# Kernel optimization log

Hardware: AMD Instinct MI355X
Metric: run time of the kernel (lower is better)

## Reference

```python
import jax, jax.numpy as jnp
import numpy as np

D_MODEL = 1024
NUM_HEADS = 16
D_K = D_MODEL // NUM_HEADS


def setup_inputs() -> dict:
    key = jax.random.key(0)
    ks = jax.random.split(key, 11)
    B, T = 4, 2048
    s = 1.0 / np.sqrt(D_MODEL)
    return {
        'query': jax.random.normal(ks[0], (B, T, D_MODEL), jnp.float32),
        'key': jax.random.normal(ks[1], (B, T, D_MODEL), jnp.float32),
        'value': jax.random.normal(ks[2], (B, T, D_MODEL), jnp.float32),
        'Wq': jax.random.normal(ks[3], (D_MODEL, D_MODEL), jnp.float32) * s,
        'bq': jnp.zeros((D_MODEL,), jnp.float32),
        'Wk': jax.random.normal(ks[4], (D_MODEL, D_MODEL), jnp.float32) * s,
        'bk': jnp.zeros((D_MODEL,), jnp.float32),
        'Wv': jax.random.normal(ks[5], (D_MODEL, D_MODEL), jnp.float32) * s,
        'bv': jnp.zeros((D_MODEL,), jnp.float32),
        'Wo': jax.random.normal(ks[6], (D_MODEL, D_MODEL), jnp.float32) * s,
        'bo': jnp.zeros((D_MODEL,), jnp.float32),
    }


def reference(query, key, value, Wq, bq, Wk, bk, Wv, bv, Wo, bo):
    B, Tq, _ = query.shape
    Tk = key.shape[1]
    # projections (torch Linear: x @ W.T + b)
    q = (query @ Wq.T + bq).reshape(B, Tq, NUM_HEADS, D_K).transpose(0, 2, 1, 3)
    k = (key @ Wk.T + bk).reshape(B, Tk, NUM_HEADS, D_K).transpose(0, 2, 1, 3)
    v = (value @ Wv.T + bv).reshape(B, Tk, NUM_HEADS, D_K).transpose(0, 2, 1, 3)
    scale = 1.0 / jnp.sqrt(jnp.asarray(D_K, q.dtype))
    scores = jnp.einsum('bhqd,bhkd->bhqk', q, k) * scale  # [B,H,Tq,Tk]
    attn = jax.nn.softmax(scores, axis=-1)
    out = jnp.einsum('bhqk,bhkd->bhqd', attn, v)
    out = out.transpose(0, 2, 1, 3).reshape(B, Tq, D_MODEL)
    return out @ Wo.T + bo
```

## Files before the change

### kernel.cpp

```cpp
#include <hip/hip_runtime.h>

typedef unsigned short u16;
typedef unsigned int u32;
typedef __attribute__((ext_vector_type(8))) short bf16x8;
typedef __attribute__((ext_vector_type(4))) float f32x4;

__device__ inline u16 f2bf(float x) {
  union { float f; unsigned u; } v; v.f = x;
  unsigned r = v.u + 0x7fffu + ((v.u >> 16) & 1u);
  return (u16)(r >> 16);
}

__device__ inline u32 packbf2(float p0, float p1) {
  return __builtin_amdgcn_perm(__float_as_uint(p1), __float_as_uint(p0), 0x07060302u);
}

__device__ inline void gload16(const void* g, void* l) {
  __builtin_amdgcn_global_load_lds(
      (const __attribute__((address_space(1))) unsigned int*)g,
      (__attribute__((address_space(3))) unsigned int*)l,
      16, 0, 0);
}

__global__ void cvt_all(const float* __restrict__ q, const float* __restrict__ k,
                        const float* __restrict__ v,
                        const float* __restrict__ wq, const float* __restrict__ wk,
                        const float* __restrict__ wv, const float* __restrict__ wo,
                        u16* __restrict__ ws) {
  const size_t MT4 = (size_t)2 * 1024 * 1024;
  const int i = blockIdx.x * blockDim.x + threadIdx.x;
  const int t = blockIdx.y;
  float4 vv;
  ushort4 o;
  if (t < 3) {
    const float* src = (t == 0) ? q : (t == 1) ? k : v;
    vv = ((const float4*)src)[i];
    o.x = f2bf(vv.x); o.y = f2bf(vv.y); o.z = f2bf(vv.z); o.w = f2bf(vv.w);
    ((ushort4*)ws)[(size_t)t * MT4 + i] = o;
  } else {
    if (i >= (1 << 20)) return;
    const int w = i >> 18, j = i & 0x3FFFF;
    const float* src = (w == 0) ? wq : (w == 1) ? wk : (w == 2) ? wv : wo;
    vv = ((const float4*)src)[j];
    o.x = f2bf(vv.x); o.y = f2bf(vv.y); o.z = f2bf(vv.z); o.w = f2bf(vv.w);
    ((ushort4*)(ws + 3 * MT4 * 4))[i] = o;
  }
}

__global__ __launch_bounds__(256, 3) void gemm_qkv(
    const u16* __restrict__ Xq, const u16* __restrict__ Wqb,
    const float* __restrict__ bq_, const float* __restrict__ bk_,
    const float* __restrict__ bv_, u16* __restrict__ Qp)
{
  constexpr int N = 1024, K = 1024, BK = 32, NT = K / BK;
  constexpr size_t MT = (size_t)8192 * 1024, WT = (size_t)1024 * 1024;
  __shared__ __align__(16) u16 As[2][128 * BK];
  __shared__ __align__(16) u16 Bs[2][128 * BK];
  const int z = blockIdx.z;
  const u16* A = Xq + (size_t)z * MT;
  const u16* W = Wqb + (size_t)z * WT;
  const float* bias = (z == 0) ? bq_ : (z == 1) ? bk_ : bv_;
  u16* Cout = Qp + (size_t)z * MT;
  const bool vm = (z == 2);

  const int tid = threadIdx.x;
  const int wave = tid >> 6, lane = tid & 63;
  const int quad = lane >> 4, l16 = lane & 15;
  const int m0 = blockIdx.x * 128, n0 = blockIdx.y * 128;

  const int sA = wave * 2;
  const int srow = lane >> 2;
  const int skcol = ((lane & 3) ^ (srow & 3)) * 8;
  const int mloc = sA * 16 + srow;
  const int arow = vm ? ((mloc & 64) + (mloc & 3) * 16 + ((mloc & 63) >> 2)) : mloc;
  const int astep = vm ? 4 : 16;
  const u16* ag = A + (size_t)(m0 + arow) * K + skcol;
  const u16* bg = W + (size_t)(n0 + mloc) * K + skcol;

  const int wm = (wave >> 1) * 64, wn = (wave & 1) * 64;
  f32x4 acc[4][4] = {};

  gload16(ag, As[0] + sA * 512);
  gload16(ag + (size_t)astep * K, As[0] + sA * 512 + 512);
  gload16(bg, Bs[0] + sA * 512);
  gload16(bg + 16 * K, Bs[0] + sA * 512 + 512);
  ag += BK; bg += BK;
  __syncthreads();

  int cur = 0;
  for (int kt = 0; kt < NT; ++kt) {
    if (kt + 1 < NT) {
      const int nb = cur ^ 1;
      gload16(ag, As[nb] + sA * 512);
      gload16(ag + (size_t)astep * K, As[nb] + sA * 512 + 512);
      gload16(bg, Bs[nb] + sA * 512);
      gload16(bg + 16 * K, Bs[nb] + sA * 512 + 512);
      ag += BK; bg += BK;
    }
    const u16* Ac = As[cur];
    const u16* Bc = Bs[cur];
    bf16x8 af[4], bf[4];
#pragma unroll
    for (int mi = 0; mi < 4; ++mi)
      af[mi] = *(const bf16x8*)(Ac + (wm + mi * 16 + l16) * BK + ((quad ^ (l16 & 3)) * 8));
#pragma unroll
    for (int ni = 0; ni < 4; ++ni)
      bf[ni] = *(const bf16x8*)(Bc + (wn + ni * 16 + l16) * BK + ((quad ^ (l16 & 3)) * 8));
#pragma unroll
    for (int mi = 0; mi < 4; ++mi)
#pragma unroll
      for (int ni = 0; ni < 4; ++ni)
        acc[mi][ni] = __builtin_amdgcn_mfma_f32_16x16x32_bf16(af[mi], bf[ni], acc[mi][ni], 0, 0, 0);
    __syncthreads();
    cur ^= 1;
  }

#pragma unroll
  for (int ni = 0; ni < 4; ++ni) {
    const int col = n0 + wn + ni * 16 + l16;
    const float bv = bias[col];
#pragma unroll
    for (int mi = 0; mi < 4; ++mi) {
      const int mrow = m0 + wm + mi * 16 + quad * 4;
      f32x4 a = acc[mi][ni];
      if (!vm) {
#pragma unroll
        for (int r = 0; r < 4; ++r)
          Cout[(size_t)(mrow + r) * N + col] = f2bf(a[r] + bv);
      } else {
        const int bq = mrow >> 11, t = mrow & 2047;
        const int h = col >> 6, d = col & 63;
        ushort4 pk;
        pk.x = f2bf(a[0] + bv); pk.y = f2bf(a[1] + bv);
        pk.z = f2bf(a[2] + bv); pk.w = f2bf(a[3] + bv);
        *(ushort4*)(Cout + ((size_t)((bq * 16 + h) * 64 + d)) * 2048 + t) = pk;
      }
    }
  }
}

template<int MODE>
__global__ __launch_bounds__(256, 2) void gemm_bt(
    const u16* __restrict__ A, const u16* __restrict__ W,
    const float* __restrict__ bias, void* __restrict__ Cout)
{
  constexpr int N = 1024, K = 1024, BK = 32, NT = K / BK;
  __shared__ __align__(16) u16 As[2][128 * BK];
  __shared__ __align__(16) u16 Bs[2][128 * BK];
  const int tid = threadIdx.x;
  const int wave = tid >> 6, lane = tid & 63;
  const int quad = lane >> 4, l16 = lane & 15;
  const int m0 = blockIdx.x * 128, n0 = blockIdx.y * 128;

  const int sA = wave * 2;
  const int srow = lane >> 2;
  const int skcol = ((lane & 3) ^ (srow & 3)) * 8;
  const int mloc = sA * 16 + srow;
  const u16* ag = A + (size_t)(m0 + mloc) * K + skcol;
  const u16* bg = W + (size_t)(n0 + mloc) * K + skcol;

  const int wm = (wave >> 1) * 64, wn = (wave & 1) * 64;
  f32x4 acc[4][4] = {};

  gload16(ag, As[0] + sA * 512);
  gload16(ag + 16 * K, As[0] + sA * 512 + 512);
  gload16(bg, Bs[0] + sA * 512);
  gload16(bg + 16 * K, Bs[0] + sA * 512 + 512);
  ag += BK; bg += BK;
  __syncthreads();

  int cur = 0;
  for (int kt = 0; kt < NT; ++kt) {
    if (kt + 1 < NT) {
      const int nb = cur ^ 1;
      gload16(ag, As[nb] + sA * 512);
      gload16(ag + 16 * K, As[nb] + sA * 512 + 512);
      gload16(bg, Bs[nb] + sA * 512);
      gload16(bg + 16 * K, Bs[nb] + sA * 512 + 512);
      ag += BK; bg += BK;
    }
    const u16* Ac = As[cur];
    const u16* Bc = Bs[cur];
    bf16x8 af[4], bf[4];
#pragma unroll
    for (int mi = 0; mi < 4; ++mi)
      af[mi] = *(const bf16x8*)(Ac + (wm + mi * 16 + l16) * BK + ((quad ^ (l16 & 3)) * 8));
#pragma unroll
    for (int ni = 0; ni < 4; ++ni)
      bf[ni] = *(const bf16x8*)(Bc + (wn + ni * 16 + l16) * BK + ((quad ^ (l16 & 3)) * 8));
#pragma unroll
    for (int mi = 0; mi < 4; ++mi)
#pragma unroll
      for (int ni = 0; ni < 4; ++ni)
        acc[mi][ni] = __builtin_amdgcn_mfma_f32_16x16x32_bf16(af[mi], bf[ni], acc[mi][ni], 0, 0, 0);
    __syncthreads();
    cur ^= 1;
  }

#pragma unroll
  for (int ni = 0; ni < 4; ++ni) {
    const int col = n0 + wn + ni * 16 + l16;
    const float bv = bias[col];
#pragma unroll
    for (int mi = 0; mi < 4; ++mi) {
      const int mrow = m0 + wm + mi * 16 + quad * 4;
      f32x4 a = acc[mi][ni];
      float* C = (float*)Cout;
#pragma unroll
      for (int r = 0; r < 4; ++r)
        C[(size_t)(mrow + r) * N + col] = a[r] + bv;
    }
  }
}

__global__ __launch_bounds__(512, 4) void flash_attn(
    const u16* __restrict__ Qp, const u16* __restrict__ Kp,
    const u16* __restrict__ Vt, u16* __restrict__ Ctx)
{
  constexpr int TQ = 2048, DM = 1024, DK = 64;
  __shared__ __align__(16) u16 Ks[2][128 * 64];
  __shared__ __align__(16) u16 Vts[2][64 * 128];
  __shared__ __align__(16) u16 Ps[8][16 * 64];

  const int bh = blockIdx.x, b = bh >> 4, h = bh & 15;
  const int qt = blockIdx.y;
  const int tid = threadIdx.x, wave = tid >> 6, lane = tid & 63;
  const int quad = lane >> 4, l16 = lane & 15;
  const int q0 = qt * 256 + wave * 32;

  const int C0 = tid, C1 = 512 + tid;
  const int kr0 = C0 >> 3, kr1 = C1 >> 3;
  const u16* kp0 = Kp + (size_t)(b * TQ + kr0) * DM + h * DK + (((C0 & 7) ^ (kr0 & 7)) * 8);
  const u16* kp1 = Kp + (size_t)(b * TQ + kr1) * DM + h * DK + (((C1 & 7) ^ (kr1 & 7)) * 8);
  const int vd0 = C0 >> 4, vd1 = C1 >> 4;
  const u16* vp0 = Vt + (size_t)(bh * DK + vd0) * TQ + (((C0 & 15) ^ (vd0 & 15)) * 8);
  const u16* vp1 = Vt + (size_t)(bh * DK + vd1) * TQ + (((C1 & 15) ^ (vd1 & 15)) * 8);

  bf16x8 qf[2][2];
#pragma unroll
  for (int mi = 0; mi < 2; ++mi)
#pragma unroll
    for (int ks = 0; ks < 2; ++ks)
      qf[mi][ks] = *(const bf16x8*)(Qp + (size_t)(b * TQ + q0 + mi * 16 + l16) * DM
                                       + h * DK + ks * 32 + quad * 8);

  f32x4 O[2][4] = {};
  f32x4 lsum[2] = {};
  const float CS = 0.18033688011112042f;
  const float CB = 0.0028153f;

  bf16x8 onesv;
#pragma unroll
  for (int j = 0; j < 8; ++j) onesv[j] = (short)0x3F80;

  gload16(kp0, &Ks[0][C0 * 8]);
  gload16(kp1, &Ks[0][C1 * 8]);
  gload16(vp0, &Vts[0][C0 * 8]);
  gload16(vp1, &Vts[0][C1 * 8]);
  kp0 += 128 * DM; kp1 += 128 * DM; vp0 += 128; vp1 += 128;
  __syncthreads();

  const int kg = quad ^ (l16 & 7);
  int cur = 0;
  for (int kt = 0; kt < TQ / 128; ++kt) {
    if (kt + 1 < TQ / 128) {
      const int nb = cur ^ 1;
      gload16(kp0, &Ks[nb][C0 * 8]);
      gload16(kp1, &Ks[nb][C1 * 8]);
      gload16(vp0, &Vts[nb][C0 * 8]);
      gload16(vp1, &Vts[nb][C1 * 8]);
      kp0 += 128 * DM; kp1 += 128 * DM; vp0 += 128; vp1 += 128;
    }
    const u16* Kc = Ks[cur];
    const u16* Vc = Vts[cur];
    u16* Psw = Ps[wave];

#pragma unroll
    for (int g = 0; g < 2; ++g) {
      f32x4 Sg[2][4];
      __builtin_amdgcn_s_setprio(1);
#pragma unroll
      for (int cc = 0; cc < 4; ++cc) {
        const int row = (g * 4 + cc) * 16 + l16;
        bf16x8 kf0 = *(const bf16x8*)(Kc + row * 64 + kg * 8);
        bf16x8 kf1 = *(const bf16x8*)(Kc + row * 64 + (kg ^ 4) * 8);
#pragma unroll
        for (int mi = 0; mi < 2; ++mi) {
          f32x4 zz = {};
          zz = __builtin_amdgcn_mfma_f32_16x16x32_bf16(qf[mi][0], kf0, zz, 0, 0, 0);
          Sg[mi][cc] = __builtin_amdgcn_mfma_f32_16x16x32_bf16(qf[mi][1], kf1, zz, 0, 0, 0);
        }
      }
      __builtin_amdgcn_s_setprio(0);
      bf16x8 pf[2][2];
#pragma unroll
      for (int mi = 0; mi < 2; ++mi) {
#pragma unroll
        for (int r = 0; r < 4; ++r) {
          float e0 = __builtin_amdgcn_exp2f(fmaf(Sg[mi][0][r], CS, CB));
          float e1 = __builtin_amdgcn_exp2f(fmaf(Sg[mi][1][r], CS, CB));
          float e2 = __builtin_amdgcn_exp2f(fmaf(Sg[mi][2][r], CS, CB));
          float e3 = __builtin_amdgcn_exp2f(fmaf(Sg[mi][3][r], CS, CB));
          uint2 pk;
          pk.x = packbf2(e0, e1);
          pk.y = packbf2(e2, e3);
          const int pw = quad * 4 + r;
          *(uint2*)(&Psw[pw * 64 + ((l16 * 4) ^ ((pw & 7) << 3))]) = pk;
        }
#pragma unroll
        for (int ksl = 0; ksl < 2; ++ksl)
          pf[mi][ksl] = *(const bf16x8*)(&Psw[l16 * 64 + ((ksl * 32 + quad * 8) ^ ((l16 & 7) << 3))]);
#pragma unroll
        for (int ksl = 0; ksl < 2; ++ksl)
          lsum[mi] = __builtin_amdgcn_mfma_f32_16x16x32_bf16(pf[mi][ksl], onesv, lsum[mi], 0, 0, 0);
      }
      __builtin_amdgcn_s_setprio(1);
#pragma unroll
      for (int ksl = 0; ksl < 2; ++ksl)
#pragma unroll
        for (int ni = 0; ni < 4; ++ni) {
          const int gv = g * 8 + ksl * 4 + quad;
          bf16x8 vf = *(const bf16x8*)(Vc + (ni * 16 + l16) * 128 + ((gv ^ l16) * 8));
          O[0][ni] = __builtin_amdgcn_mfma_f32_16x16x32_bf16(pf[0][ksl], vf, O[0][ni], 0, 0, 0);
          O[1][ni] = __builtin_amdgcn_mfma_f32_16x16x32_bf16(pf[1][ksl], vf, O[1][ni], 0, 0, 0);
        }
      __builtin_amdgcn_s_setprio(0);
    }
    __syncthreads();
    cur ^= 1;
  }

#pragma unroll
  for (int mi = 0; mi < 2; ++mi)
#pragma unroll
    for (int r = 0; r < 4; ++r) {
      const float inv = 1.0f / lsum[mi][r];
      const int q = q0 + mi * 16 + quad * 4 + r;
#pragma unroll
      for (int ni = 0; ni < 4; ++ni) {
        const int col = h * DK + ni * 16 + l16;
        Ctx[(size_t)(b * TQ + q) * DM + col] = f2bf(O[mi][ni][r] * inv);
      }
    }
}

extern "C" void kernel_launch(void* const* d_in, const int* in_sizes, int n_in,
                              void* d_out, int out_size, void* d_ws, size_t ws_size,
                              hipStream_t stream)
{
  (void)in_sizes; (void)n_in; (void)out_size; (void)ws_size;
  const float* query = (const float*)d_in[0];
  const float* key_  = (const float*)d_in[1];
  const float* value = (const float*)d_in[2];
  const float* Wq = (const float*)d_in[3];
  const float* bq = (const float*)d_in[4];
  const float* Wk = (const float*)d_in[5];
  const float* bk = (const float*)d_in[6];
  const float* Wv = (const float*)d_in[7];
  const float* bv = (const float*)d_in[8];
  const float* Wo = (const float*)d_in[9];
  const float* bo = (const float*)d_in[10];

  const size_t MT = (size_t)4 * 2048 * 1024;
  const size_t WT = (size_t)1024 * 1024;
  u16* ws  = (u16*)d_ws;
  u16* Xq  = ws;
  u16* Wqb = Xq + 3 * MT;
  u16* Qp  = Wqb + 4 * WT;
  u16* Kp  = Qp + MT;
  u16* Vt  = Kp + MT;
  u16* Ctx = Vt + MT;
  u16* Wob = Wqb + 3 * WT;

  cvt_all<<<dim3(8192, 4), 256, 0, stream>>>(
      query, key_, value, Wq, Wk, Wv, Wo, ws);

  gemm_qkv<<<dim3(64, 8, 3), 256, 0, stream>>>(Xq, Wqb, bq, bk, bv, Qp);

  flash_attn<<<dim3(64, 8), 512, 0, stream>>>(Qp, Kp, Vt, Ctx);

  gemm_bt<2><<<dim3(64, 8), 256, 0, stream>>>(Ctx, Wob, bo, (float*)d_out);
}
```

Before: 341.3 us.

## Triple-buffer LDS in projection GEMMs with explicit vmcnt waits and single barrier

Both the QKV projection GEMM and the output projection GEMM move from double-buffered to triple-buffered LDS tiles, prefetching two K-steps ahead. Each iteration now uses a partial s_waitcnt vmcnt and one s_barrier in place of a full __syncthreads at the end of every step. The goal is to keep more global-to-LDS loads in flight and to remove one barrier per iteration. The cost is 50% more LDS per block, which could lower occupancy (the QKV kernel requests 3 blocks per CU). The hand-written waitcnt also depends on the compiler not emitting other vector memory ops inside the loop.

```diff
diff --git a/kernel.cpp b/kernel.cpp
--- a/kernel.cpp
+++ b/kernel.cpp
@@ -54,8 +54,8 @@
 {
   constexpr int N = 1024, K = 1024, BK = 32, NT = K / BK;
   constexpr size_t MT = (size_t)8192 * 1024, WT = (size_t)1024 * 1024;
-  __shared__ __align__(16) u16 As[2][128 * BK];
-  __shared__ __align__(16) u16 Bs[2][128 * BK];
+  __shared__ __align__(16) u16 As[3][128 * BK];
+  __shared__ __align__(16) u16 Bs[3][128 * BK];
   const int z = blockIdx.z;
   const u16* A = Xq + (size_t)z * MT;
   const u16* W = Wqb + (size_t)z * WT;
@@ -80,25 +80,31 @@
   const int wm = (wave >> 1) * 64, wn = (wave & 1) * 64;
   f32x4 acc[4][4] = {};
 
-  gload16(ag, As[0] + sA * 512);
-  gload16(ag + (size_t)astep * K, As[0] + sA * 512 + 512);
-  gload16(bg, Bs[0] + sA * 512);
-  gload16(bg + 16 * K, Bs[0] + sA * 512 + 512);
-  ag += BK; bg += BK;
-  __syncthreads();
-
-  int cur = 0;
+#define QKV_STAGE(s)                                   \
+  do {                                                 \
+    gload16(ag, As[s] + sA * 512);                     \
+    gload16(ag + (size_t)astep * K, As[s] + sA * 512 + 512); \
+    gload16(bg, Bs[s] + sA * 512);                     \
+    gload16(bg + 16 * K, Bs[s] + sA * 512 + 512);      \
+    ag += BK; bg += BK;                                \
+  } while (0)
+
+  QKV_STAGE(0);
+  QKV_STAGE(1);
+
+  int cb = 0, sb = 2;
   for (int kt = 0; kt < NT; ++kt) {
-    if (kt + 1 < NT) {
-      const int nb = cur ^ 1;
-      gload16(ag, As[nb] + sA * 512);
-      gload16(ag + (size_t)astep * K, As[nb] + sA * 512 + 512);
-      gload16(bg, Bs[nb] + sA * 512);
-      gload16(bg + 16 * K, Bs[nb] + sA * 512 + 512);
-      ag += BK; bg += BK;
-    }
-    const u16* Ac = As[cur];
-    const u16* Bc = Bs[cur];
+    if (kt + 1 < NT) asm volatile("s_waitcnt vmcnt(4)" ::: "memory");
+    else             asm volatile("s_waitcnt vmcnt(0)" ::: "memory");
+    __builtin_amdgcn_s_barrier();
+    __builtin_amdgcn_sched_barrier(0);
+    if (kt + 2 < NT) {
+      QKV_STAGE(sb);
+      sb = (sb == 2) ? 0 : sb + 1;
+    }
+    const u16* Ac = As[cb];
+    const u16* Bc = Bs[cb];
+    cb = (cb == 2) ? 0 : cb + 1;
     bf16x8 af[4], bf[4];
 #pragma unroll
     for (int mi = 0; mi < 4; ++mi)
@@ -111,9 +117,8 @@
 #pragma unroll
       for (int ni = 0; ni < 4; ++ni)
         acc[mi][ni] = __builtin_amdgcn_mfma_f32_16x16x32_bf16(af[mi], bf[ni], acc[mi][ni], 0, 0, 0);
-    __syncthreads();
-    cur ^= 1;
-  }
+  }
+#undef QKV_STAGE
 
 #pragma unroll
   for (int ni = 0; ni < 4; ++ni) {
@@ -139,14 +144,13 @@
   }
 }
 
-template<int MODE>
-__global__ __launch_bounds__(256, 2) void gemm_bt(
+__global__ __launch_bounds__(256, 2) void gemm_wo(
     const u16* __restrict__ A, const u16* __restrict__ W,
-    const float* __restrict__ bias, void* __restrict__ Cout)
+    const float* __restrict__ bias, float* __restrict__ Cout)
 {
   constexpr int N = 1024, K = 1024, BK = 32, NT = K / BK;
-  __shared__ __align__(16) u16 As[2][128 * BK];
-  __shared__ __align__(16) u16 Bs[2][128 * BK];
+  __shared__ __align__(16) u16 As[3][128 * BK];
+  __shared__ __align__(16) u16 Bs[3][128 * BK];
   const int tid = threadIdx.x;
   const int wave = tid >> 6, lane = tid & 63;
   const int quad = lane >> 4, l16 = lane & 15;
@@ -162,25 +166,31 @@
   const int wm = (wave >> 1) * 64, wn = (wave & 1) * 64;
   f32x4 acc[4][4] = {};
 
-  gload16(ag, As[0] + sA * 512);
-  gload16(ag + 16 * K, As[0] + sA * 512 + 512);
-  gload16(bg, Bs[0] + sA * 512);
-  gload16(bg + 16 * K, Bs[0] + sA * 512 + 512);
-  ag += BK; bg += BK;
-  __syncthreads();
-
-  int cur = 0;
+#define WO_STAGE(s)                                    \
+  do {                                                 \
+    gload16(ag, As[s] + sA * 512);                     \
+    gload16(ag + 16 * K, As[s] + sA * 512 + 512);      \
+    gload16(bg, Bs[s] + sA * 512);                     \
+    gload16(bg + 16 * K, Bs[s] + sA * 512 + 512);      \
+    ag += BK; bg += BK;                                \
+  } while (0)
+
+  WO_STAGE(0);
+  WO_STAGE(1);
+
+  int cb = 0, sb = 2;
   for (int kt = 0; kt < NT; ++kt) {
-    if (kt + 1 < NT) {
-      const int nb = cur ^ 1;
-      gload16(ag, As[nb] + sA * 512);
-      gload16(ag + 16 * K, As[nb] + sA * 512 + 512);
-      gload16(bg, Bs[nb] + sA * 512);
-      gload16(bg + 16 * K, Bs[nb] + sA * 512 + 512);
-      ag += BK; bg += BK;
-    }
-    const u16* Ac = As[cur];
-    const u16* Bc = Bs[cur];
+    if (kt + 1 < NT) asm volatile("s_waitcnt vmcnt(4)" ::: "memory");
+    else             asm volatile("s_waitcnt vmcnt(0)" ::: "memory");
+    __builtin_amdgcn_s_barrier();
+    __builtin_amdgcn_sched_barrier(0);
+    if (kt + 2 < NT) {
+      WO_STAGE(sb);
+      sb = (sb == 2) ? 0 : sb + 1;
+    }
+    const u16* Ac = As[cb];
+    const u16* Bc = Bs[cb];
+    cb = (cb == 2) ? 0 : cb + 1;
     bf16x8 af[4], bf[4];
 #pragma unroll
     for (int mi = 0; mi < 4; ++mi)
@@ -193,9 +203,8 @@
 #pragma unroll
       for (int ni = 0; ni < 4; ++ni)
         acc[mi][ni] = __builtin_amdgcn_mfma_f32_16x16x32_bf16(af[mi], bf[ni], acc[mi][ni], 0, 0, 0);
-    __syncthreads();
-    cur ^= 1;
-  }
+  }
+#undef WO_STAGE
 
 #pragma unroll
   for (int ni = 0; ni < 4; ++ni) {
@@ -205,10 +214,9 @@
     for (int mi = 0; mi < 4; ++mi) {
       const int mrow = m0 + wm + mi * 16 + quad * 4;
       f32x4 a = acc[mi][ni];
-      float* C = (float*)Cout;
 #pragma unroll
       for (int r = 0; r < 4; ++r)
-        C[(size_t)(mrow + r) * N + col] = a[r] + bv;
+        Cout[(size_t)(mrow + r) * N + col] = a[r] + bv;
     }
   }
 }
@@ -379,5 +387,5 @@
 
   flash_attn<<<dim3(64, 8), 512, 0, stream>>>(Qp, Kp, Vt, Ctx);
 
-  gemm_bt<2><<<dim3(64, 8), 256, 0, stream>>>(Ctx, Wob, bo, (float*)d_out);
-}
+  gemm_wo<<<dim3(64, 8), 256, 0, stream>>>(Ctx, Wob, bo, (float*)d_out);
+}
```

Measured after the change: 328.1 us. 1.04x faster.
